# Kernel optimization log

Hardware: AMD Instinct MI355X
Metric: run time of the kernel (lower is better)

Reference implementation:

```python
import jax, jax.numpy as jnp
import numpy as np

B, N, C = 16, 1024, 768            # N = window_size**2 = 32*32
NUM_HEADS, BANK = 12, 256
HEAD_DIM = C // NUM_HEADS
LN_EPS = 1e-5


def setup_inputs() -> dict:
    key = jax.random.key(0)
    ks = jax.random.split(key, 9)
    s = 0.02
    return {
        "x": jax.random.normal(ks[0], (B, N, C), dtype=jnp.float32),
        "qkv_w": jax.random.normal(ks[1], (3 * C, C), dtype=jnp.float32) * s,
        "qkv_b": jnp.zeros((3 * C,), dtype=jnp.float32),
        "proj_w": jax.random.normal(ks[2], (C, C), dtype=jnp.float32) * s,
        "proj_b": jnp.zeros((C,), dtype=jnp.float32),
        "norm_w": jnp.ones((C,), dtype=jnp.float32),
        "norm_b": jnp.zeros((C,), dtype=jnp.float32),
        "bank_k": jax.random.normal(ks[3], (BANK, C), dtype=jnp.float32) * s,
        "bank_v": jax.random.normal(ks[4], (BANK, C), dtype=jnp.float32) * s,
    }


def _split_heads_bank(bank, b):
    # (BANK, C) -> broadcast to (b, BANK, C) -> (b, H, BANK, D)
    t = jnp.broadcast_to(bank, (b,) + bank.shape)
    return t.reshape(b, BANK, NUM_HEADS, HEAD_DIM).transpose(0, 2, 1, 3)


def reference(x, qkv_w, qkv_b, proj_w, proj_b, norm_w, norm_b, bank_k, bank_v):
    b, n, c = x.shape
    h, d = NUM_HEADS, HEAD_DIM
    # QKV projection: (b, n, 3c) -> (3, b, h, n, d)
    qkv = (jnp.einsum("bnc,fc->bnf", x, qkv_w) + qkv_b)
    qkv = qkv.reshape(b, n, 3, h, d).transpose(2, 0, 3, 1, 4)
    q, k, v = qkv[0], qkv[1], qkv[2]
    # Memory-bank read + concat onto KV
    k_full = jnp.concatenate([k, _split_heads_bank(bank_k, b)], axis=2)  # (b,h,n+BANK,d)
    v_full = jnp.concatenate([v, _split_heads_bank(bank_v, b)], axis=2)
    # SDPA (dropout_p = 0.0)
    scores = jnp.einsum("bhnd,bhmd->bhnm", q, k_full) / jnp.sqrt(jnp.asarray(d, x.dtype))
    attn = jax.nn.softmax(scores, axis=-1)
    out = jnp.einsum("bhnm,bhmd->bhnd", attn, v_full)
    out = out.transpose(0, 2, 1, 3).reshape(b, n, c)
    # Bank write value: LayerNorm(proj(out))  (side effect in torch; returned here)
    p = jnp.einsum("bnc,oc->bno", out, proj_w) + proj_b
    mu = jnp.mean(p, axis=-1, keepdims=True)
    var = jnp.mean(jnp.square(p - mu), axis=-1, keepdims=True)
    bank_update = (p - mu) * jax.lax.rsqrt(var + LN_EPS) * norm_w + norm_b
    return out, bank_update
```

## Files before the change

kernel.cpp:

```cpp
#include <hip/hip_runtime.h>

typedef __attribute__((ext_vector_type(8))) short short8;
typedef __attribute__((ext_vector_type(4))) float float4_t;
typedef unsigned short u16;

#define K_DIM 768

__device__ __forceinline__ u16 f2bf(float f) {
  union { float f; unsigned u; } v; v.f = f;
  unsigned r = v.u + 0x7FFFu + ((v.u >> 16) & 1u);
  return (u16)(r >> 16);
}

__device__ __forceinline__ u16 f2bf_trunc(float f) {
  union { float f; unsigned u; } v; v.f = f;
  return (u16)(v.u >> 16);
}

__device__ __forceinline__ void gload16(const void* g, void* l) {
  __builtin_amdgcn_global_load_lds(
      (__attribute__((address_space(1))) void*)g,
      (__attribute__((address_space(3))) void*)l, 16, 0, 0);
}

__global__ __launch_bounds__(256) void cvt_all_kernel(
    const float* __restrict__ x, const float* __restrict__ qw,
    const float* __restrict__ pw, const float* __restrict__ bkf,
    const float* __restrict__ bvf,
    u16* __restrict__ xbf, u16* __restrict__ qwbf, u16* __restrict__ pwbf,
    u16* __restrict__ bk, u16* __restrict__ bvt) {
  const int blk = blockIdx.x;
  if (blk < 14592) {
    int i = blk * 256 + threadIdx.x;
    const float* src; u16* dst;
    if (i < 3145728)      { src = x;  dst = xbf; }
    else if (i < 3588096) { src = qw; dst = qwbf; i -= 3145728; }
    else                  { src = pw; dst = pwbf; i -= 3588096; }
    float4 v = ((const float4*)src)[i];
    union { u16 h[4]; unsigned long long ll; } o;
    o.h[0] = f2bf(v.x); o.h[1] = f2bf(v.y); o.h[2] = f2bf(v.z); o.h[3] = f2bf(v.w);
    ((unsigned long long*)dst)[i] = o.ll;
  } else {
    int idx = (blk - 14592) * 256 + threadIdx.x;
    int m = idx / 768;
    int c = idx - m * 768;
    int h = c >> 6, d = c & 63;
    bk[(h * 256 + m) * 64 + d] = f2bf(bkf[idx]);
    bvt[(h * 64 + d) * 256 + m] = f2bf(bvf[idx]);
  }
}

template <int MODE>
__global__ __launch_bounds__(256) void gemm128b(
    const u16* __restrict__ A, const u16* __restrict__ Bw,
    const float* __restrict__ bias,
    u16* __restrict__ q_ws, u16* __restrict__ k_ws, u16* __restrict__ vt_ws,
    float* __restrict__ p_out) {
  __shared__ u16 As[2][8192];
  __shared__ u16 Bs[2][8192];
  const int tid = threadIdx.x;
  const int w = tid >> 6, lane = tid & 63;
  const int l15 = lane & 15, quad = lane >> 4;
  const int wm = w >> 1, wn = w & 1;

  constexpr int NBN = (MODE == 0) ? 18 : 6;
  const int bid = blockIdx.x;
  const int xcd = bid & 7, local = bid >> 3;
  const int bm = xcd * 16 + local / NBN;
  const int bn = local % NBN;

  int soff[4], loff[4];
#pragma unroll
  for (int r = 0; r < 4; r++) {
    const int off = r * 4096 + tid * 16;
    const int row = off >> 7;
    const int grp = (off & 127) >> 4;
    soff[r] = row * K_DIM + (grp ^ (row & 7)) * 8;
    loff[r] = off;
  }
  const u16* Abase = A + (size_t)bm * 128 * K_DIM;
  const u16* Bbase = Bw + (size_t)bn * 128 * K_DIM;

  auto stg = [&](const u16* g0, u16* l0, int kt) {
#pragma unroll
    for (int r = 0; r < 4; r++)
      gload16(g0 + soff[r] + kt, (char*)l0 + loff[r]);
  };

  const int ab0 = l15 * 128 + ((quad ^ (l15 & 7)) << 4);
  const int ab1 = l15 * 128 + (((4 + quad) ^ (l15 & 7)) << 4);

  float4_t acc[4][4];
#pragma unroll
  for (int i = 0; i < 4; i++)
#pragma unroll
    for (int j = 0; j < 4; j++) acc[i][j] = (float4_t){0.f, 0.f, 0.f, 0.f};

  stg(Abase, As[0], 0);
  stg(Bbase, Bs[0], 0);
  __syncthreads();

  int buf = 0;
#pragma unroll 1
  for (int t = 0; t < 12; t++) {
    if (t < 11) {
      stg(Abase, As[buf ^ 1], (t + 1) * 64);
      stg(Bbase, Bs[buf ^ 1], (t + 1) * 64);
    }
    short8 af[4][2], bfr[4][2];
#pragma unroll
    for (int mt = 0; mt < 4; mt++) {
      const char* p = (const char*)As[buf] + ((wm * 64 + mt * 16) << 7);
      af[mt][0] = *(const short8*)(p + ab0);
      af[mt][1] = *(const short8*)(p + ab1);
    }
#pragma unroll
    for (int nt = 0; nt < 4; nt++) {
      const char* p = (const char*)Bs[buf] + ((wn * 64 + nt * 16) << 7);
      bfr[nt][0] = *(const short8*)(p + ab0);
      bfr[nt][1] = *(const short8*)(p + ab1);
    }
#pragma unroll
    for (int mt = 0; mt < 4; mt++)
#pragma unroll
      for (int nt = 0; nt < 4; nt++) {
        acc[mt][nt] = __builtin_amdgcn_mfma_f32_16x16x32_bf16(
            af[mt][0], bfr[nt][0], acc[mt][nt], 0, 0, 0);
        acc[mt][nt] = __builtin_amdgcn_mfma_f32_16x16x32_bf16(
            af[mt][1], bfr[nt][1], acc[mt][nt], 0, 0, 0);
      }
    __syncthreads();
    buf ^= 1;
  }

  const float QS = 0.18033688011112042f;
#pragma unroll
  for (int mt = 0; mt < 4; mt++) {
#pragma unroll
    for (int nt = 0; nt < 4; nt++) {
      const int row0 = bm * 128 + wm * 64 + mt * 16 + quad * 4;
      const int f = bn * 128 + wn * 64 + nt * 16 + l15;
      const float bv = bias[f];
      if (MODE == 0) {
        const int which = f / 768;
        const int rem = f - which * 768;
        const int h = rem >> 6, d = rem & 63;
#pragma unroll
        for (int r2 = 0; r2 < 4; r2++) {
          float v = acc[mt][nt][r2] + bv;
          const int i = row0 + r2;
          const int bb = i >> 10, n = i & 1023;
          const size_t bhh = (size_t)(bb * 12 + h);
          if (which == 0)      q_ws[(bhh * 1024 + n) * 64 + d] = f2bf(v * QS);
          else if (which == 1) k_ws[(bhh * 1024 + n) * 64 + d] = f2bf(v);
          else                 vt_ws[(bhh * 64 + d) * 1024 + n] = f2bf(v);
        }
      } else {
#pragma unroll
        for (int r2 = 0; r2 < 4; r2++) {
          const int i = row0 + r2;
          p_out[(size_t)i * 768 + f] = acc[mt][nt][r2] + bv;
        }
      }
    }
  }
}

__global__ __launch_bounds__(256) void fa_kernel(
    const u16* __restrict__ qws, const u16* __restrict__ kws,
    const u16* __restrict__ vtws, const u16* __restrict__ bk,
    const u16* __restrict__ bvt,
    float* __restrict__ out, u16* __restrict__ obf) {
  __shared__ u16 smem[2][8192];

  const int tid = threadIdx.x;
  const int w = tid >> 6, lane = tid & 63;
  const int l15 = lane & 15, quad = lane >> 4;
  const int bh = blockIdx.x;
  const int b = bh / 12, h = bh - b * 12;
  const int q0 = blockIdx.y * 128 + w * 32;

  short8 qf[2][2];
  {
    const u16* qb = qws + ((size_t)bh * 1024 + q0) * 64;
#pragma unroll
    for (int rt = 0; rt < 2; rt++)
#pragma unroll
      for (int c = 0; c < 2; c++)
        qf[rt][c] = *(const short8*)(qb + (rt * 16 + l15) * 64 + c * 32 + quad * 8);
  }

  const short ONE = (short)0x3F80;
  const short8 onesf = (short8){ONE, ONE, ONE, ONE, ONE, ONE, ONE, ONE};

  float4_t O[2][4];
  float4_t lacc[2];
#pragma unroll
  for (int rt = 0; rt < 2; rt++) {
#pragma unroll
    for (int dt = 0; dt < 4; dt++) O[rt][dt] = (float4_t){0.f, 0.f, 0.f, 0.f};
    lacc[rt] = (float4_t){0.f, 0.f, 0.f, 0.f};
  }

  auto stage = [&](int tt, int buf) {
    const int mb = tt * 64;
    u16* Ksb = &smem[buf][0];
    u16* Vtb = &smem[buf][4096];
#pragma unroll
    for (int r = 0; r < 2; r++) {
      const int off = (w * 2 + r) * 1024 + lane * 16;
      const int row = off >> 7;
      const int grp = (off & 127) >> 4;
      const int lcol = (grp ^ (row & 7)) * 8;
      const u16* g = (mb < 1024)
          ? kws + ((size_t)bh * 1024 + mb + row) * 64 + lcol
          : bk + ((size_t)h * 256 + (mb - 1024) + row) * 64 + lcol;
      gload16(g, (char*)Ksb + off);
      const u16* g2 = (mb < 1024)
          ? vtws + ((size_t)bh * 64 + row) * 1024 + mb + lcol
          : bvt + ((size_t)h * 64 + row) * 256 + (mb - 1024) + lcol;
      gload16(g2, (char*)Vtb + off);
    }
  };

  stage(0, 0);
  __builtin_amdgcn_sched_barrier(0);
  asm volatile("s_waitcnt vmcnt(0)" ::: "memory");
  __builtin_amdgcn_s_barrier();
  __builtin_amdgcn_sched_barrier(0);

#pragma unroll 1
  for (int t = 0; t < 20; t++) {
    const int cur = t & 1;
    if (t < 19) stage(t + 1, cur ^ 1);

    const u16* Ks  = &smem[cur][0];
    const u16* Vts = &smem[cur][4096];
    u16* Psw = &smem[cur][0] + w * 2048;

    short8 kf[4][2];
#pragma unroll
    for (int ct = 0; ct < 4; ct++)
#pragma unroll
      for (int c = 0; c < 2; c++) {
        const int row = ct * 16 + l15;
        kf[ct][c] = *(const short8*)(Ks + row * 64 + ((c * 4 + quad) ^ (row & 7)) * 8);
      }

    float4_t S[2][4];
#pragma unroll
    for (int rt = 0; rt < 2; rt++)
#pragma unroll
      for (int ct = 0; ct < 4; ct++) {
        float4_t z = (float4_t){0.f, 0.f, 0.f, 0.f};
        z = __builtin_amdgcn_mfma_f32_16x16x32_bf16(qf[rt][0], kf[ct][0], z, 0, 0, 0);
        S[rt][ct] = __builtin_amdgcn_mfma_f32_16x16x32_bf16(qf[rt][1], kf[ct][1], z, 0, 0, 0);
      }

    short8 vf[4][2];
#pragma unroll
    for (int dt = 0; dt < 4; dt++)
#pragma unroll
      for (int c = 0; c < 2; c++) {
        const int row = dt * 16 + l15;
        vf[dt][c] = *(const short8*)(Vts + row * 64 + ((c * 4 + quad) ^ (row & 7)) * 8);
      }

    __builtin_amdgcn_sched_barrier(0);
    asm volatile("s_waitcnt lgkmcnt(0)" ::: "memory");
    __builtin_amdgcn_s_barrier();
    __builtin_amdgcn_sched_barrier(0);

#pragma unroll
    for (int rt = 0; rt < 2; rt++) {
#pragma unroll
      for (int ct = 0; ct < 4; ct++) {
        const int colg = ct * 2 + (l15 >> 3);
#pragma unroll
        for (int r = 0; r < 4; r++) {
          const float p = __builtin_amdgcn_exp2f(S[rt][ct][r]);
          const int q = rt * 16 + quad * 4 + r;
          Psw[q * 64 + (colg ^ (q & 7)) * 8 + (l15 & 7)] = f2bf_trunc(p);
        }
      }
    }

#pragma unroll
    for (int rt = 0; rt < 2; rt++)
#pragma unroll
      for (int c = 0; c < 2; c++) {
        const int qrow = rt * 16 + l15;
        const short8 pf = *(const short8*)(&Psw[qrow * 64 + (((c * 4 + quad) ^ (qrow & 7)) * 8)]);
#pragma unroll
        for (int dt = 0; dt < 4; dt++)
          O[rt][dt] = __builtin_amdgcn_mfma_f32_16x16x32_bf16(pf, vf[dt][c], O[rt][dt], 0, 0, 0);
        lacc[rt] = __builtin_amdgcn_mfma_f32_16x16x32_bf16(pf, onesf, lacc[rt], 0, 0, 0);
      }

    __builtin_amdgcn_sched_barrier(0);
    asm volatile("s_waitcnt vmcnt(0) lgkmcnt(0)" ::: "memory");
    __builtin_amdgcn_s_barrier();
    __builtin_amdgcn_sched_barrier(0);
  }

#pragma unroll
  for (int rt = 0; rt < 2; rt++) {
    float rl[4];
#pragma unroll
    for (int r = 0; r < 4; r++) rl[r] = 1.f / lacc[rt][r];
#pragma unroll
    for (int dt = 0; dt < 4; dt++)
#pragma unroll
      for (int r = 0; r < 4; r++) {
        const float v = O[rt][dt][r] * rl[r];
        const int n = q0 + rt * 16 + quad * 4 + r;
        const int d = dt * 16 + l15;
        const size_t idx = ((size_t)b * 1024 + n) * 768 + h * 64 + d;
        out[idx] = v;
        obf[idx] = f2bf(v);
      }
  }
}

__global__ __launch_bounds__(256) void ln_kernel(float* __restrict__ p,
                                                 const float* __restrict__ nw,
                                                 const float* __restrict__ nb) {
  __shared__ float red[2][4];
  const int row = blockIdx.x, tid = threadIdx.x;
  float* pr = p + (size_t)row * 768;
  const float x0 = pr[tid], x1 = pr[tid + 256], x2 = pr[tid + 512];
  float s = x0 + x1 + x2;
  float sq = x0 * x0 + x1 * x1 + x2 * x2;
#pragma unroll
  for (int m = 1; m < 64; m <<= 1) {
    s += __shfl_xor(s, m, 64);
    sq += __shfl_xor(sq, m, 64);
  }
  const int w = tid >> 6;
  if ((tid & 63) == 0) { red[0][w] = s; red[1][w] = sq; }
  __syncthreads();
  s = red[0][0] + red[0][1] + red[0][2] + red[0][3];
  sq = red[1][0] + red[1][1] + red[1][2] + red[1][3];
  const float mean = s * (1.0f / 768.0f);
  const float var = sq * (1.0f / 768.0f) - mean * mean;
  const float rstd = rsqrtf(var + 1e-5f);
  pr[tid]       = (x0 - mean) * rstd * nw[tid]       + nb[tid];
  pr[tid + 256] = (x1 - mean) * rstd * nw[tid + 256] + nb[tid + 256];
  pr[tid + 512] = (x2 - mean) * rstd * nw[tid + 512] + nb[tid + 512];
}

extern "C" void kernel_launch(void* const* d_in, const int* in_sizes, int n_in,
                              void* d_out, int out_size, void* d_ws, size_t ws_size,
                              hipStream_t stream) {
  (void)in_sizes; (void)n_in; (void)out_size; (void)ws_size;
  const float* x      = (const float*)d_in[0];
  const float* qkv_w  = (const float*)d_in[1];
  const float* qkv_b  = (const float*)d_in[2];
  const float* proj_w = (const float*)d_in[3];
  const float* proj_b = (const float*)d_in[4];
  const float* norm_w = (const float*)d_in[5];
  const float* norm_b = (const float*)d_in[6];
  const float* bank_k = (const float*)d_in[7];
  const float* bank_v = (const float*)d_in[8];

  char* ws = (char*)d_ws;
  u16* xbf   = (u16*)(ws + 0);
  u16* obf   = (u16*)(ws + 0);
  u16* qwbf  = (u16*)(ws + 25165824);
  u16* pwbf  = (u16*)(ws + 28704768);
  u16* bkbf  = (u16*)(ws + 29884416);
  u16* bvtbf = (u16*)(ws + 30277632);
  u16* q_ws  = (u16*)(ws + 30670848);
  u16* k_ws  = (u16*)(ws + 55836672);
  u16* vt_ws = (u16*)(ws + 81002496);

  float* out0  = (float*)d_out;
  float* p_out = out0 + 12582912;

  cvt_all_kernel<<<15360, 256, 0, stream>>>(x, qkv_w, proj_w, bank_k, bank_v,
                                            xbf, qwbf, pwbf, bkbf, bvtbf);

  gemm128b<0><<<dim3(2304), 256, 0, stream>>>(xbf, qwbf, qkv_b, q_ws, k_ws, vt_ws, nullptr);
  fa_kernel<<<dim3(192, 8), 256, 0, stream>>>(q_ws, k_ws, vt_ws, bkbf, bvtbf, out0, obf);
  gemm128b<1><<<dim3(768), 256, 0, stream>>>(obf, pwbf, proj_b, nullptr, nullptr, nullptr, p_out);
  ln_kernel<<<16384, 256, 0, stream>>>(p_out, norm_w, norm_b);
}
```

Baseline: 400.7 us.

## Enlarge GEMM tiles to 256x256 with 512 threads and K-step 32

```diff
diff --git a/kernel.cpp b/kernel.cpp
--- a/kernel.cpp
+++ b/kernel.cpp
@@ -51,7 +51,7 @@
 }
 
 template <int MODE>
-__global__ __launch_bounds__(256) void gemm128b(
+__global__ __launch_bounds__(512) void gemm256b(
     const u16* __restrict__ A, const u16* __restrict__ Bw,
     const float* __restrict__ bias,
     u16* __restrict__ q_ws, u16* __restrict__ k_ws, u16* __restrict__ vt_ws,
@@ -61,38 +61,37 @@
   const int tid = threadIdx.x;
   const int w = tid >> 6, lane = tid & 63;
   const int l15 = lane & 15, quad = lane >> 4;
-  const int wm = w >> 1, wn = w & 1;
-
-  constexpr int NBN = (MODE == 0) ? 18 : 6;
+  const int wm = w >> 2, wn = w & 3;
+
+  constexpr int NBN = (MODE == 0) ? 9 : 3;
   const int bid = blockIdx.x;
   const int xcd = bid & 7, local = bid >> 3;
-  const int bm = xcd * 16 + local / NBN;
+  const int bm = xcd * 8 + local / NBN;
   const int bn = local % NBN;
 
-  int soff[4], loff[4];
-#pragma unroll
-  for (int r = 0; r < 4; r++) {
-    const int off = r * 4096 + tid * 16;
-    const int row = off >> 7;
-    const int grp = (off & 127) >> 4;
-    soff[r] = row * K_DIM + (grp ^ (row & 7)) * 8;
+  int soff[2], loff[2];
+#pragma unroll
+  for (int r = 0; r < 2; r++) {
+    const int off = r * 8192 + tid * 16;
+    const int row = off >> 6;
+    const int grp = (off & 63) >> 4;
+    soff[r] = row * K_DIM + (grp ^ ((row >> 1) & 3)) * 8;
     loff[r] = off;
   }
-  const u16* Abase = A + (size_t)bm * 128 * K_DIM;
-  const u16* Bbase = Bw + (size_t)bn * 128 * K_DIM;
+  const u16* Abase = A + (size_t)bm * 256 * K_DIM;
+  const u16* Bbase = Bw + (size_t)bn * 256 * K_DIM;
 
   auto stg = [&](const u16* g0, u16* l0, int kt) {
 #pragma unroll
-    for (int r = 0; r < 4; r++)
+    for (int r = 0; r < 2; r++)
       gload16(g0 + soff[r] + kt, (char*)l0 + loff[r]);
   };
 
-  const int ab0 = l15 * 128 + ((quad ^ (l15 & 7)) << 4);
-  const int ab1 = l15 * 128 + (((4 + quad) ^ (l15 & 7)) << 4);
-
-  float4_t acc[4][4];
-#pragma unroll
-  for (int i = 0; i < 4; i++)
+  const int ab = l15 * 64 + ((quad ^ ((l15 >> 1) & 3)) << 4);
+
+  float4_t acc[8][4];
+#pragma unroll
+  for (int i = 0; i < 8; i++)
 #pragma unroll
     for (int j = 0; j < 4; j++) acc[i][j] = (float4_t){0.f, 0.f, 0.f, 0.f};
 
@@ -102,44 +101,37 @@
 
   int buf = 0;
 #pragma unroll 1
-  for (int t = 0; t < 12; t++) {
-    if (t < 11) {
-      stg(Abase, As[buf ^ 1], (t + 1) * 64);
-      stg(Bbase, Bs[buf ^ 1], (t + 1) * 64);
+  for (int t = 0; t < 24; t++) {
+    if (t < 23) {
+      stg(Abase, As[buf ^ 1], (t + 1) * 32);
+      stg(Bbase, Bs[buf ^ 1], (t + 1) * 32);
     }
-    short8 af[4][2], bfr[4][2];
-#pragma unroll
-    for (int mt = 0; mt < 4; mt++) {
-      const char* p = (const char*)As[buf] + ((wm * 64 + mt * 16) << 7);
-      af[mt][0] = *(const short8*)(p + ab0);
-      af[mt][1] = *(const short8*)(p + ab1);
-    }
-#pragma unroll
-    for (int nt = 0; nt < 4; nt++) {
-      const char* p = (const char*)Bs[buf] + ((wn * 64 + nt * 16) << 7);
-      bfr[nt][0] = *(const short8*)(p + ab0);
-      bfr[nt][1] = *(const short8*)(p + ab1);
-    }
-#pragma unroll
-    for (int mt = 0; mt < 4; mt++)
-#pragma unroll
-      for (int nt = 0; nt < 4; nt++) {
+    short8 af[8], bfr[4];
+#pragma unroll
+    for (int mt = 0; mt < 8; mt++)
+      af[mt] = *(const short8*)((const char*)As[buf] +
+                                ((wm * 128 + mt * 16) << 6) + ab);
+#pragma unroll
+    for (int nt = 0; nt < 4; nt++)
+      bfr[nt] = *(const short8*)((const char*)Bs[buf] +
+                                 ((wn * 64 + nt * 16) << 6) + ab);
+#pragma unroll
+    for (int mt = 0; mt < 8; mt++)
+#pragma unroll
+      for (int nt = 0; nt < 4; nt++)
         acc[mt][nt] = __builtin_amdgcn_mfma_f32_16x16x32_bf16(
-            af[mt][0], bfr[nt][0], acc[mt][nt], 0, 0, 0);
-        acc[mt][nt] = __builtin_amdgcn_mfma_f32_16x16x32_bf16(
-            af[mt][1], bfr[nt][1], acc[mt][nt], 0, 0, 0);
-      }
+            af[mt], bfr[nt], acc[mt][nt], 0, 0, 0);
     __syncthreads();
     buf ^= 1;
   }
 
   const float QS = 0.18033688011112042f;
 #pragma unroll
-  for (int mt = 0; mt < 4; mt++) {
-#pragma unroll
-    for (int nt = 0; nt < 4; nt++) {
-      const int row0 = bm * 128 + wm * 64 + mt * 16 + quad * 4;
-      const int f = bn * 128 + wn * 64 + nt * 16 + l15;
+  for (int mi = 0; mi < 8; mi++) {
+#pragma unroll
+    for (int ni = 0; ni < 4; ni++) {
+      const int row0 = bm * 256 + wm * 128 + mi * 16 + quad * 4;
+      const int f = bn * 256 + wn * 64 + ni * 16 + l15;
       const float bv = bias[f];
       if (MODE == 0) {
         const int which = f / 768;
@@ -147,7 +139,7 @@
         const int h = rem >> 6, d = rem & 63;
 #pragma unroll
         for (int r2 = 0; r2 < 4; r2++) {
-          float v = acc[mt][nt][r2] + bv;
+          float v = acc[mi][ni][r2] + bv;
           const int i = row0 + r2;
           const int bb = i >> 10, n = i & 1023;
           const size_t bhh = (size_t)(bb * 12 + h);
@@ -159,7 +151,7 @@
 #pragma unroll
         for (int r2 = 0; r2 < 4; r2++) {
           const int i = row0 + r2;
-          p_out[(size_t)i * 768 + f] = acc[mt][nt][r2] + bv;
+          p_out[(size_t)i * 768 + f] = acc[mi][ni][r2] + bv;
         }
       }
     }
@@ -380,8 +372,8 @@
   cvt_all_kernel<<<15360, 256, 0, stream>>>(x, qkv_w, proj_w, bank_k, bank_v,
                                             xbf, qwbf, pwbf, bkbf, bvtbf);
 
-  gemm128b<0><<<dim3(2304), 256, 0, stream>>>(xbf, qwbf, qkv_b, q_ws, k_ws, vt_ws, nullptr);
+  gemm256b<0><<<dim3(576), 512, 0, stream>>>(xbf, qwbf, qkv_b, q_ws, k_ws, vt_ws, nullptr);
   fa_kernel<<<dim3(192, 8), 256, 0, stream>>>(q_ws, k_ws, vt_ws, bkbf, bvtbf, out0, obf);
-  gemm128b<1><<<dim3(768), 256, 0, stream>>>(obf, pwbf, proj_b, nullptr, nullptr, nullptr, p_out);
+  gemm256b<1><<<dim3(192), 512, 0, stream>>>(obf, pwbf, proj_b, nullptr, nullptr, nullptr, p_out);
   ln_kernel<<<16384, 256, 0, stream>>>(p_out, norm_w, norm_b);
 }
```

Result: slower. 432.7 us (+8.0%).

## Triple-buffer GEMM with K-tile 32 and explicit waitcnt-based pipelining

Applied to the files above, without the earlier changes.

```diff
diff --git a/kernel.cpp b/kernel.cpp
--- a/kernel.cpp
+++ b/kernel.cpp
@@ -51,13 +51,13 @@
 }
 
 template <int MODE>
-__global__ __launch_bounds__(256) void gemm128b(
+__global__ __launch_bounds__(256) void gemm128c(
     const u16* __restrict__ A, const u16* __restrict__ Bw,
     const float* __restrict__ bias,
     u16* __restrict__ q_ws, u16* __restrict__ k_ws, u16* __restrict__ vt_ws,
     float* __restrict__ p_out) {
-  __shared__ u16 As[2][8192];
-  __shared__ u16 Bs[2][8192];
+  __shared__ u16 As[3][4096];
+  __shared__ u16 Bs[3][4096];
   const int tid = threadIdx.x;
   const int w = tid >> 6, lane = tid & 63;
   const int l15 = lane & 15, quad = lane >> 4;
@@ -69,13 +69,13 @@
   const int bm = xcd * 16 + local / NBN;
   const int bn = local % NBN;
 
-  int soff[4], loff[4];
-#pragma unroll
-  for (int r = 0; r < 4; r++) {
+  int soff[2], loff[2];
+#pragma unroll
+  for (int r = 0; r < 2; r++) {
     const int off = r * 4096 + tid * 16;
-    const int row = off >> 7;
-    const int grp = (off & 127) >> 4;
-    soff[r] = row * K_DIM + (grp ^ (row & 7)) * 8;
+    const int row = off >> 6;
+    const int grp = (off & 63) >> 4;
+    soff[r] = row * K_DIM + (grp ^ ((row >> 1) & 3)) * 8;
     loff[r] = off;
   }
   const u16* Abase = A + (size_t)bm * 128 * K_DIM;
@@ -83,12 +83,11 @@
 
   auto stg = [&](const u16* g0, u16* l0, int kt) {
 #pragma unroll
-    for (int r = 0; r < 4; r++)
+    for (int r = 0; r < 2; r++)
       gload16(g0 + soff[r] + kt, (char*)l0 + loff[r]);
   };
 
-  const int ab0 = l15 * 128 + ((quad ^ (l15 & 7)) << 4);
-  const int ab1 = l15 * 128 + (((4 + quad) ^ (l15 & 7)) << 4);
+  const int ab = l15 * 64 + ((quad ^ ((l15 >> 1) & 3)) << 4);
 
   float4_t acc[4][4];
 #pragma unroll
@@ -96,42 +95,54 @@
 #pragma unroll
     for (int j = 0; j < 4; j++) acc[i][j] = (float4_t){0.f, 0.f, 0.f, 0.f};
 
-  stg(Abase, As[0], 0);
-  stg(Bbase, Bs[0], 0);
-  __syncthreads();
-
-  int buf = 0;
+  u16 *a0 = As[0], *a1 = As[1], *a2 = As[2];
+  u16 *b0 = Bs[0], *b1 = Bs[1], *b2 = Bs[2];
+
+  auto compute = [&](const u16* ar, const u16* br) {
+    short8 af[4], bfr[4];
+#pragma unroll
+    for (int mt = 0; mt < 4; mt++)
+      af[mt] = *(const short8*)((const char*)ar + ((wm * 64 + mt * 16) << 6) + ab);
+#pragma unroll
+    for (int nt = 0; nt < 4; nt++)
+      bfr[nt] = *(const short8*)((const char*)br + ((wn * 64 + nt * 16) << 6) + ab);
+#pragma unroll
+    for (int mt = 0; mt < 4; mt++)
+#pragma unroll
+      for (int nt = 0; nt < 4; nt++)
+        acc[mt][nt] = __builtin_amdgcn_mfma_f32_16x16x32_bf16(
+            af[mt], bfr[nt], acc[mt][nt], 0, 0, 0);
+  };
+
+  stg(Abase, a0, 0);  stg(Bbase, b0, 0);
+  stg(Abase, a1, 32); stg(Bbase, b1, 32);
+
 #pragma unroll 1
-  for (int t = 0; t < 12; t++) {
-    if (t < 11) {
-      stg(Abase, As[buf ^ 1], (t + 1) * 64);
-      stg(Bbase, Bs[buf ^ 1], (t + 1) * 64);
-    }
-    short8 af[4][2], bfr[4][2];
-#pragma unroll
-    for (int mt = 0; mt < 4; mt++) {
-      const char* p = (const char*)As[buf] + ((wm * 64 + mt * 16) << 7);
-      af[mt][0] = *(const short8*)(p + ab0);
-      af[mt][1] = *(const short8*)(p + ab1);
-    }
-#pragma unroll
-    for (int nt = 0; nt < 4; nt++) {
-      const char* p = (const char*)Bs[buf] + ((wn * 64 + nt * 16) << 7);
-      bfr[nt][0] = *(const short8*)(p + ab0);
-      bfr[nt][1] = *(const short8*)(p + ab1);
-    }
-#pragma unroll
-    for (int mt = 0; mt < 4; mt++)
-#pragma unroll
-      for (int nt = 0; nt < 4; nt++) {
-        acc[mt][nt] = __builtin_amdgcn_mfma_f32_16x16x32_bf16(
-            af[mt][0], bfr[nt][0], acc[mt][nt], 0, 0, 0);
-        acc[mt][nt] = __builtin_amdgcn_mfma_f32_16x16x32_bf16(
-            af[mt][1], bfr[nt][1], acc[mt][nt], 0, 0, 0);
-      }
-    __syncthreads();
-    buf ^= 1;
-  }
+  for (int t = 0; t < 22; t++) {
+    __builtin_amdgcn_sched_barrier(0);
+    asm volatile("s_waitcnt lgkmcnt(0)" ::: "memory");
+    __builtin_amdgcn_s_barrier();
+    __builtin_amdgcn_sched_barrier(0);
+    stg(Abase, a2, (t + 2) * 32);
+    stg(Bbase, b2, (t + 2) * 32);
+    __builtin_amdgcn_sched_barrier(0);
+    asm volatile("s_waitcnt vmcnt(8)" ::: "memory");
+    __builtin_amdgcn_s_barrier();
+    __builtin_amdgcn_sched_barrier(0);
+    compute(a0, b0);
+    u16* ta = a0; a0 = a1; a1 = a2; a2 = ta;
+    u16* tb = b0; b0 = b1; b1 = b2; b2 = tb;
+  }
+  __builtin_amdgcn_sched_barrier(0);
+  asm volatile("s_waitcnt vmcnt(4)" ::: "memory");
+  __builtin_amdgcn_s_barrier();
+  __builtin_amdgcn_sched_barrier(0);
+  compute(a0, b0);
+  __builtin_amdgcn_sched_barrier(0);
+  asm volatile("s_waitcnt vmcnt(0)" ::: "memory");
+  __builtin_amdgcn_s_barrier();
+  __builtin_amdgcn_sched_barrier(0);
+  compute(a1, b1);
 
   const float QS = 0.18033688011112042f;
 #pragma unroll
@@ -380,8 +391,8 @@
   cvt_all_kernel<<<15360, 256, 0, stream>>>(x, qkv_w, proj_w, bank_k, bank_v,
                                             xbf, qwbf, pwbf, bkbf, bvtbf);
 
-  gemm128b<0><<<dim3(2304), 256, 0, stream>>>(xbf, qwbf, qkv_b, q_ws, k_ws, vt_ws, nullptr);
+  gemm128c<0><<<dim3(2304), 256, 0, stream>>>(xbf, qwbf, qkv_b, q_ws, k_ws, vt_ws, nullptr);
   fa_kernel<<<dim3(192, 8), 256, 0, stream>>>(q_ws, k_ws, vt_ws, bkbf, bvtbf, out0, obf);
-  gemm128b<1><<<dim3(768), 256, 0, stream>>>(obf, pwbf, proj_b, nullptr, nullptr, nullptr, p_out);
+  gemm128c<1><<<dim3(768), 256, 0, stream>>>(obf, pwbf, proj_b, nullptr, nullptr, nullptr, p_out);
   ln_kernel<<<16384, 256, 0, stream>>>(p_out, norm_w, norm_b);
 }
```

After: 404.9 us. About the same (+1.1%).
